# Optimization experiments

Measured on AMD Instinct MI355X. Metric: run time of the kernel, lower is better.

Reference implementation:

```python
import jax, jax.numpy as jnp
import numpy as np

CLASS_COST = 2.0
BBOX_COST = 5.0
GIOU_COST = 2.0
ALPHA = 0.25
GAMMA = 2.0
EPS = 1e-08


def center_to_corners(b):
    # b: [..., 4] in (cx, cy, w, h) -> (x0, y0, x1, y1)
    cx, cy, w, h = b[..., 0], b[..., 1], b[..., 2], b[..., 3]
    return jnp.stack([cx - 0.5 * w, cy - 0.5 * h, cx + 0.5 * w, cy + 0.5 * h], axis=-1)


def generalized_box_iou(boxes1, boxes2):
    # boxes1: [N,4], boxes2: [M,4], corners format -> [N,M] GIoU
    area1 = (boxes1[:, 2] - boxes1[:, 0]) * (boxes1[:, 3] - boxes1[:, 1])
    area2 = (boxes2[:, 2] - boxes2[:, 0]) * (boxes2[:, 3] - boxes2[:, 1])
    lt = jnp.maximum(boxes1[:, None, :2], boxes2[None, :, :2])  # [N,M,2]
    rb = jnp.minimum(boxes1[:, None, 2:], boxes2[None, :, 2:])
    wh = jnp.clip(rb - lt, 0.0)
    inter = wh[..., 0] * wh[..., 1]  # [N,M]
    union = area1[:, None] + area2[None, :] - inter
    iou = inter / union
    lt_e = jnp.minimum(boxes1[:, None, :2], boxes2[None, :, :2])
    rb_e = jnp.maximum(boxes1[:, None, 2:], boxes2[None, :, 2:])
    wh_e = jnp.clip(rb_e - lt_e, 0.0)
    area_e = wh_e[..., 0] * wh_e[..., 1]
    return iou - (area_e - union) / area_e


def setup_inputs() -> dict:
    key = jax.random.key(0)
    k1, k2, k3, k4, k5 = jax.random.split(key, 5)
    B, Q, C, T, L = 16, 900, 512, 40, 91
    return {
        "logits": jax.random.normal(k1, (B, Q, C), dtype=jnp.float32),
        "pred_boxes": jax.random.uniform(k2, (B, Q, 4), dtype=jnp.float32),
        "label_maps": jax.random.uniform(k3, (B, L, C), dtype=jnp.float32),
        "boxes": jax.random.uniform(k4, (B, T, 4), dtype=jnp.float32),
        "class_labels": jax.random.randint(k5, (B, T), 0, L, dtype=jnp.int32),
    }


def reference(logits, pred_boxes, label_maps, boxes, class_labels):
    B, Q, C = logits.shape
    T = boxes.shape[1]
    out_prob = jax.nn.sigmoid(logits.reshape(B * Q, C))          # [BQ, C]
    out_bbox = pred_boxes.reshape(B * Q, 4)
    # gather per-batch label maps, then normalize
    lm = jax.vmap(lambda m, idx: m[idx])(label_maps, class_labels)  # [B, T, C]
    lm = lm.reshape(B * T, C)
    lm = lm / lm.sum(axis=-1, keepdims=True)
    target_bbox = boxes.reshape(B * T, 4)
    # focal-style class cost
    neg_cost = (1 - ALPHA) * out_prob ** GAMMA * (-jnp.log(1 - out_prob + EPS))
    pos_cost = ALPHA * (1 - out_prob) ** GAMMA * (-jnp.log(out_prob + EPS))
    class_cost = (pos_cost - neg_cost) @ lm.T                    # [BQ, BT]
    bbox_cost = jnp.sum(jnp.abs(out_bbox[:, None, :] - target_bbox[None, :, :]), axis=-1)
    giou_cost = -generalized_box_iou(center_to_corners(out_bbox), center_to_corners(target_bbox))
    cost = BBOX_COST * bbox_cost + CLASS_COST * class_cost + GIOU_COST * giou_cost
    return cost.reshape(B, Q, B * T)
```

## Files before the change

kernel.cpp:

```cpp
#include <hip/hip_runtime.h>
#include <hip/hip_bf16.h>

#define BQ   14400
#define BT   640
#define CD   512
#define LD   91
#define TD   40

typedef __attribute__((ext_vector_type(8))) short short8;
typedef __attribute__((ext_vector_type(4))) float f32x4;

__global__ __launch_bounds__(256) void build_lmfrag_kernel(
    const float* __restrict__ label_maps,
    const int* __restrict__ class_labels,
    __hip_bfloat16* __restrict__ Bf)
{
    __shared__ float rows[16][512];
    __shared__ float inv[16];
    int nt = blockIdx.x;
    int t  = threadIdx.x;

    #pragma unroll
    for (int e = 0; e < 8; ++e) {
        int idx4 = t + e * 256;
        int r    = idx4 >> 7;
        int c4   = idx4 & 127;
        int j    = nt * 16 + r;
        int b    = j / TD;
        int cls  = class_labels[j];
        float4 v = *(const float4*)(label_maps + ((size_t)(b * LD + cls) * CD) + c4 * 4);
        *(float4*)(&rows[r][c4 * 4]) = v;
    }
    __syncthreads();

    int w = t >> 6, l = t & 63;
    #pragma unroll
    for (int q = 0; q < 4; ++q) {
        int r = w * 4 + q;
        float s = 0.f;
        #pragma unroll
        for (int e = 0; e < 8; ++e) s += rows[r][l + e * 64];
        #pragma unroll
        for (int off = 32; off >= 1; off >>= 1) s += __shfl_down(s, off, 64);
        if (l == 0) inv[r] = __builtin_amdgcn_rcpf(s);
    }
    __syncthreads();

    #pragma unroll
    for (int e = 0; e < 4; ++e) {
        int sc = t + e * 256;
        int kb = sc >> 6;
        int ln = sc & 63;
        int o  = ln >> 4;
        int rr = ln & 15;
        float scale = inv[rr];
        union { __hip_bfloat16 h[8]; uint4 u; } pk;
        #pragma unroll
        for (int j2 = 0; j2 < 8; ++j2)
            pk.h[j2] = __float2bfloat16(rows[rr][kb * 32 + o * 8 + j2] * scale);
        *(uint4*)((char*)Bf + ((size_t)nt * 1024 + sc) * 16) = pk.u;
    }
}

__device__ __forceinline__ float focal_term(float x)
{
    x = fminf(fmaxf(x, -18.0f), 18.0f);
    float q   = __expf(-x);
    float s   = 1.0f + q;
    float p   = __builtin_amdgcn_rcpf(s);
    float spn = __logf(s);
    float omp = q * p;
    float pos = 0.25f * omp * omp * spn;
    float neg = 0.75f * p * p * (x + spn);
    return pos - neg;
}

__global__ __launch_bounds__(512, 2) void fused_cost_kernel(
    const float* __restrict__ logits,
    const float* __restrict__ pred_boxes,
    const __hip_bfloat16* __restrict__ Bf,
    const float* __restrict__ tboxes,
    float* __restrict__ out)
{
    __shared__ __align__(16) short A[64][512];
    __shared__ float pB[64][4];
    __shared__ float tB[BT][4];

    int t  = threadIdx.x;
    int m0 = blockIdx.x * 64;

    if (t < 64)  *(float4*)(&pB[t][0]) = *(const float4*)(pred_boxes + (size_t)(m0 + t) * 4);
    *(float4*)(&tB[t][0]) = *(const float4*)(tboxes + (size_t)t * 4);
    if (t < BT - 512) *(float4*)(&tB[512 + t][0]) = *(const float4*)(tboxes + (size_t)(512 + t) * 4);

    {
        int row = t >> 3;
        int sl  = t & 7;
        int r7  = row & 7;
        const float* lp = logits + (size_t)(m0 + row) * CD + sl * 16;
        #pragma unroll
        for (int i = 0; i < 4; ++i) {
            union { float4 v4[4]; float f[16]; } xu;
            #pragma unroll
            for (int j = 0; j < 4; ++j) xu.v4[j] = *(const float4*)(lp + i * 128 + j * 4);
            union { __hip_bfloat16 h[16]; uint4 u[2]; } pk;
            #pragma unroll
            for (int k = 0; k < 16; ++k) pk.h[k] = __float2bfloat16(focal_term(xu.f[k]));
            int o0 = sl * 2 + i * 16;
            *(uint4*)(&A[row][(o0 ^ r7) * 8])       = pk.u[0];
            *(uint4*)(&A[row][((o0 + 1) ^ r7) * 8]) = pk.u[1];
        }
    }
    __syncthreads();

    int l    = t & 63;
    int w    = t >> 6;
    int wr   = w & 1;
    int wcg  = w >> 1;
    int lrow = l & 15;
    int kg   = l >> 4;
    int r7a  = lrow & 7;
    int arow0 = wr * 32 + lrow;
    int arow1 = arow0 + 16;

    f32x4 acc[2][10] = {};
    const short8* bp = (const short8*)Bf + (size_t)wcg * 10240 + l;

    #pragma unroll 2
    for (int kb = 0; kb < 16; ++kb) {
        short8 a0 = *(const short8*)(&A[arow0][((kb * 4 + kg) ^ r7a) * 8]);
        short8 a1 = *(const short8*)(&A[arow1][((kb * 4 + kg) ^ r7a) * 8]);
        short8 bfr[10];
        #pragma unroll
        for (int nf = 0; nf < 10; ++nf) bfr[nf] = bp[nf * 1024 + kb * 64];
        #pragma unroll
        for (int nf = 0; nf < 10; ++nf) {
            acc[0][nf] = __builtin_amdgcn_mfma_f32_16x16x32_bf16(a0, bfr[nf], acc[0][nf], 0, 0, 0);
            acc[1][nf] = __builtin_amdgcn_mfma_f32_16x16x32_bf16(a1, bfr[nf], acc[1][nf], 0, 0, 0);
        }
    }

    float rp[8][9];
    #pragma unroll
    for (int rf = 0; rf < 2; ++rf) {
        #pragma unroll
        for (int r = 0; r < 4; ++r) {
            int rl = wr * 32 + rf * 16 + kg * 4 + r;
            float pcx = pB[rl][0], pcy = pB[rl][1], pw = pB[rl][2], ph = pB[rl][3];
            float* P = rp[rf * 4 + r];
            P[0] = pcx; P[1] = pcy; P[2] = pw; P[3] = ph;
            P[4] = pcx - 0.5f * pw;
            P[5] = pcy - 0.5f * ph;
            P[6] = pcx + 0.5f * pw;
            P[7] = pcy + 0.5f * ph;
            P[8] = pw * ph;
        }
    }

    #pragma unroll
    for (int nf = 0; nf < 10; ++nf) {
        int cl = wcg * 160 + nf * 16 + lrow;
        float tcx = tB[cl][0], tcy = tB[cl][1], tw = tB[cl][2], th = tB[cl][3];
        float tx0 = tcx - 0.5f * tw, ty0 = tcy - 0.5f * th;
        float tx1 = tcx + 0.5f * tw, ty1 = tcy + 0.5f * th;
        float areaT = tw * th;
        #pragma unroll
        for (int rf = 0; rf < 2; ++rf) {
            #pragma unroll
            for (int r = 0; r < 4; ++r) {
                const float* P = rp[rf * 4 + r];
                float bbox = fabsf(P[0] - tcx) + fabsf(P[1] - tcy)
                           + fabsf(P[2] - tw)  + fabsf(P[3] - th);
                float iw = fminf(P[6], tx1) - fmaxf(P[4], tx0);
                float ih = fminf(P[7], ty1) - fmaxf(P[5], ty0);
                iw = fmaxf(iw, 0.0f); ih = fmaxf(ih, 0.0f);
                float inter = iw * ih;
                float uni   = P[8] + areaT - inter;
                float ew = fmaxf(P[6], tx1) - fminf(P[4], tx0);
                float eh = fmaxf(P[7], ty1) - fminf(P[5], ty0);
                float areaE = ew * eh;
                float iou  = inter * __builtin_amdgcn_rcpf(uni);
                float gpen = (areaE - uni) * __builtin_amdgcn_rcpf(areaE);
                float giou = iou - gpen;
                float cls  = acc[rf][nf][r];
                int rl = wr * 32 + rf * 16 + kg * 4 + r;
                out[(size_t)(m0 + rl) * BT + cl] = 5.0f * bbox + 2.0f * cls - 2.0f * giou;
            }
        }
    }
}

extern "C" void kernel_launch(void* const* d_in, const int* in_sizes, int n_in,
                              void* d_out, int out_size, void* d_ws, size_t ws_size,
                              hipStream_t stream) {
    const float* logits       = (const float*)d_in[0];
    const float* pred_boxes   = (const float*)d_in[1];
    const float* label_maps   = (const float*)d_in[2];
    const float* boxes        = (const float*)d_in[3];
    const int*   class_labels = (const int*)d_in[4];
    float* out = (float*)d_out;

    __hip_bfloat16* Bf = (__hip_bfloat16*)d_ws;

    build_lmfrag_kernel<<<40, 256, 0, stream>>>(label_maps, class_labels, Bf);
    fused_cost_kernel<<<BQ / 64, 512, 0, stream>>>(logits, pred_boxes, Bf, boxes, out);
}
```

Measured before the change: 120.4 us.

## Remap wave tiling to 64x80 per wave with prefetched B fragments

Changes the MFMA work split so each wave covers all 64 rows and an 80-column slice instead of 32x160, and reorders the label-map fragment buffer so each wave's data is contiguous per k-step. B fragments are triple-buffered in registers, with the first two k-steps loaded before the logit/focal prologue, so global load latency overlaps with the A-tile computation. Target boxes are read directly from global into registers rather than staged in shared memory, and the epilogue loops over rows first. The idea is to hide B-load latency and cut redundant B traffic, at the cost of more register pressure and fewer rows reused per B fragment.

```diff
diff --git a/kernel.cpp b/kernel.cpp
--- a/kernel.cpp
+++ b/kernel.cpp
@@ -46,6 +46,7 @@
     }
     __syncthreads();
 
+    int w5 = nt / 5, nf5 = nt % 5;
     #pragma unroll
     for (int e = 0; e < 4; ++e) {
         int sc = t + e * 256;
@@ -58,7 +59,8 @@
         #pragma unroll
         for (int j2 = 0; j2 < 8; ++j2)
             pk.h[j2] = __float2bfloat16(rows[rr][kb * 32 + o * 8 + j2] * scale);
-        *(uint4*)((char*)Bf + ((size_t)nt * 1024 + sc) * 16) = pk.u;
+        size_t chunk = (size_t)(w5 * 16 + kb) * 5 + nf5;
+        *(uint4*)((char*)Bf + (chunk * 64 + ln) * 16) = pk.u;
     }
 }
 
@@ -84,14 +86,24 @@
 {
     __shared__ __align__(16) short A[64][512];
     __shared__ float pB[64][4];
-    __shared__ float tB[BT][4];
 
     int t  = threadIdx.x;
     int m0 = blockIdx.x * 64;
-
-    if (t < 64)  *(float4*)(&pB[t][0]) = *(const float4*)(pred_boxes + (size_t)(m0 + t) * 4);
-    *(float4*)(&tB[t][0]) = *(const float4*)(tboxes + (size_t)t * 4);
-    if (t < BT - 512) *(float4*)(&tB[512 + t][0]) = *(const float4*)(tboxes + (size_t)(512 + t) * 4);
+    int l    = t & 63;
+    int w    = t >> 6;
+    int lrow = l & 15;
+    int kg   = l >> 4;
+    int r7a  = lrow & 7;
+
+    const short8* bw = (const short8*)Bf + (size_t)w * 80 * 64 + l;
+
+    short8 b0[5], b1[5], b2[5];
+    #pragma unroll
+    for (int nf = 0; nf < 5; ++nf) b0[nf] = bw[(0 * 5 + nf) * 64];
+    #pragma unroll
+    for (int nf = 0; nf < 5; ++nf) b1[nf] = bw[(1 * 5 + nf) * 64];
+
+    if (t < 64) *(float4*)(&pB[t][0]) = *(const float4*)(pred_boxes + (size_t)(m0 + t) * 4);
 
     {
         int row = t >> 3;
@@ -113,78 +125,65 @@
     }
     __syncthreads();
 
-    int l    = t & 63;
-    int w    = t >> 6;
-    int wr   = w & 1;
-    int wcg  = w >> 1;
-    int lrow = l & 15;
-    int kg   = l >> 4;
-    int r7a  = lrow & 7;
-    int arow0 = wr * 32 + lrow;
-    int arow1 = arow0 + 16;
-
-    f32x4 acc[2][10] = {};
-    const short8* bp = (const short8*)Bf + (size_t)wcg * 10240 + l;
-
-    #pragma unroll 2
+    f32x4 acc[4][5] = {};
+    #pragma unroll
     for (int kb = 0; kb < 16; ++kb) {
-        short8 a0 = *(const short8*)(&A[arow0][((kb * 4 + kg) ^ r7a) * 8]);
-        short8 a1 = *(const short8*)(&A[arow1][((kb * 4 + kg) ^ r7a) * 8]);
-        short8 bfr[10];
-        #pragma unroll
-        for (int nf = 0; nf < 10; ++nf) bfr[nf] = bp[nf * 1024 + kb * 64];
-        #pragma unroll
-        for (int nf = 0; nf < 10; ++nf) {
-            acc[0][nf] = __builtin_amdgcn_mfma_f32_16x16x32_bf16(a0, bfr[nf], acc[0][nf], 0, 0, 0);
-            acc[1][nf] = __builtin_amdgcn_mfma_f32_16x16x32_bf16(a1, bfr[nf], acc[1][nf], 0, 0, 0);
-        }
-    }
-
-    float rp[8][9];
-    #pragma unroll
-    for (int rf = 0; rf < 2; ++rf) {
+        short8* const bufs[3] = { b0, b1, b2 };
+        if (kb < 14) {
+            short8* nb = bufs[(kb + 2) % 3];
+            #pragma unroll
+            for (int nf = 0; nf < 5; ++nf) nb[nf] = bw[((kb + 2) * 5 + nf) * 64];
+        }
+        const short8* cb = bufs[kb % 3];
+        #pragma unroll
+        for (int rf = 0; rf < 4; ++rf) {
+            short8 a = *(const short8*)(&A[rf * 16 + lrow][((kb * 4 + kg) ^ r7a) * 8]);
+            #pragma unroll
+            for (int nf = 0; nf < 5; ++nf)
+                acc[rf][nf] = __builtin_amdgcn_mfma_f32_16x16x32_bf16(a, cb[nf], acc[rf][nf], 0, 0, 0);
+        }
+    }
+
+    float tc[5][8];
+    #pragma unroll
+    for (int nf = 0; nf < 5; ++nf) {
+        int cl = w * 80 + nf * 16 + lrow;
+        float4 tb = *(const float4*)(tboxes + (size_t)cl * 4);
+        tc[nf][0] = tb.x; tc[nf][1] = tb.y; tc[nf][2] = tb.z; tc[nf][3] = tb.w;
+        tc[nf][4] = tb.x - 0.5f * tb.z;
+        tc[nf][5] = tb.y - 0.5f * tb.w;
+        tc[nf][6] = tb.x + 0.5f * tb.z;
+        tc[nf][7] = tb.y + 0.5f * tb.w;
+    }
+
+    #pragma unroll
+    for (int rf = 0; rf < 4; ++rf) {
         #pragma unroll
         for (int r = 0; r < 4; ++r) {
-            int rl = wr * 32 + rf * 16 + kg * 4 + r;
-            float pcx = pB[rl][0], pcy = pB[rl][1], pw = pB[rl][2], ph = pB[rl][3];
-            float* P = rp[rf * 4 + r];
-            P[0] = pcx; P[1] = pcy; P[2] = pw; P[3] = ph;
-            P[4] = pcx - 0.5f * pw;
-            P[5] = pcy - 0.5f * ph;
-            P[6] = pcx + 0.5f * pw;
-            P[7] = pcy + 0.5f * ph;
-            P[8] = pw * ph;
-        }
-    }
-
-    #pragma unroll
-    for (int nf = 0; nf < 10; ++nf) {
-        int cl = wcg * 160 + nf * 16 + lrow;
-        float tcx = tB[cl][0], tcy = tB[cl][1], tw = tB[cl][2], th = tB[cl][3];
-        float tx0 = tcx - 0.5f * tw, ty0 = tcy - 0.5f * th;
-        float tx1 = tcx + 0.5f * tw, ty1 = tcy + 0.5f * th;
-        float areaT = tw * th;
-        #pragma unroll
-        for (int rf = 0; rf < 2; ++rf) {
-            #pragma unroll
-            for (int r = 0; r < 4; ++r) {
-                const float* P = rp[rf * 4 + r];
-                float bbox = fabsf(P[0] - tcx) + fabsf(P[1] - tcy)
-                           + fabsf(P[2] - tw)  + fabsf(P[3] - th);
-                float iw = fminf(P[6], tx1) - fmaxf(P[4], tx0);
-                float ih = fminf(P[7], ty1) - fmaxf(P[5], ty0);
+            int rl = rf * 16 + kg * 4 + r;
+            float4 pb = *(const float4*)(&pB[rl][0]);
+            float px0 = pb.x - 0.5f * pb.z, py0 = pb.y - 0.5f * pb.w;
+            float px1 = pb.x + 0.5f * pb.z, py1 = pb.y + 0.5f * pb.w;
+            float areaP = pb.z * pb.w;
+            size_t orow = (size_t)(m0 + rl) * BT + w * 80 + lrow;
+            #pragma unroll
+            for (int nf = 0; nf < 5; ++nf) {
+                const float* T = tc[nf];
+                float bbox = fabsf(pb.x - T[0]) + fabsf(pb.y - T[1])
+                           + fabsf(pb.z - T[2]) + fabsf(pb.w - T[3]);
+                float iw = fminf(px1, T[6]) - fmaxf(px0, T[4]);
+                float ih = fminf(py1, T[7]) - fmaxf(py0, T[5]);
                 iw = fmaxf(iw, 0.0f); ih = fmaxf(ih, 0.0f);
                 float inter = iw * ih;
-                float uni   = P[8] + areaT - inter;
-                float ew = fmaxf(P[6], tx1) - fminf(P[4], tx0);
-                float eh = fmaxf(P[7], ty1) - fminf(P[5], ty0);
+                float uni   = areaP + T[2] * T[3] - inter;
+                float ew = fmaxf(px1, T[6]) - fminf(px0, T[4]);
+                float eh = fmaxf(py1, T[7]) - fminf(py0, T[5]);
                 float areaE = ew * eh;
                 float iou  = inter * __builtin_amdgcn_rcpf(uni);
                 float gpen = (areaE - uni) * __builtin_amdgcn_rcpf(areaE);
                 float giou = iou - gpen;
                 float cls  = acc[rf][nf][r];
-                int rl = wr * 32 + rf * 16 + kg * 4 + r;
-                out[(size_t)(m0 + rl) * BT + cl] = 5.0f * bbox + 2.0f * cls - 2.0f * giou;
+                out[orow + nf * 16] = 5.0f * bbox + 2.0f * cls - 2.0f * giou;
             }
         }
     }
```

Measured after the change: 109.4 us. -9.2%, faster.
